# Kernel tuning notes

Hardware: AMD Instinct MI355X
Metric: run time of the kernel (lower is better)

## Reference

```python
import jax, jax.numpy as jnp
import numpy as np

WS = [2048, 4096, 8192]
RS = [1, 2, 4]
OFFSET = 0
NEG = -1e30


def _causal_attn(xseg, Wq, Wk, Wv, Wo):
    """xseg: (b, s, m, c). Returns (out (b,s,m,c), denom (b,s,m)) where denom is
    the softmax denominator sum_j exp(score_ij) per query (computed stably via lse)."""
    c = xseg.shape[-1]
    m = xseg.shape[-2]
    q = jnp.einsum('bsmc,cd->bsmd', xseg, Wq)
    k = jnp.einsum('bsmc,cd->bsmd', xseg, Wk)
    v = jnp.einsum('bsmc,cd->bsmd', xseg, Wv)
    scores = jnp.einsum('bsid,bsjd->bsij', q, k) / jnp.sqrt(jnp.asarray(c, xseg.dtype))
    causal = jnp.tril(jnp.ones((m, m), dtype=bool))
    scores = jnp.where(causal, scores, NEG)
    lse = jax.nn.logsumexp(scores, axis=-1)            # (b,s,m)
    p = jnp.exp(scores - lse[..., None])               # softmax
    o = jnp.einsum('bsij,bsjd->bsid', p, v)
    o = jnp.einsum('bsid,dc->bsic', o, Wo)
    return o, jnp.exp(lse)


def setup_inputs() -> dict:
    key = jax.random.key(0)
    kx, kq, kk, kv, ko = jax.random.split(key, 5)
    b, n, c = 4, 8192, 128
    scale = 1.0 / np.sqrt(c)  # keep activations O(1) so exp(lse) stays finite
    return {
        'x': jax.random.normal(kx, (b, n, c), dtype=jnp.float32),
        'Wq': jax.random.normal(kq, (c, c), dtype=jnp.float32) * scale,
        'Wk': jax.random.normal(kk, (c, c), dtype=jnp.float32) * scale,
        'Wv': jax.random.normal(kv, (c, c), dtype=jnp.float32) * scale,
        'Wo': jax.random.normal(ko, (c, c), dtype=jnp.float32) * scale,
    }


def reference(x, Wq, Wk, Wv, Wo):
    b, n, c = x.shape
    denom_sums = jnp.zeros((b, n), dtype=x.dtype)
    branches = []
    for w, r in zip(WS, RS):
        s = n // w
        # gather dilated tokens within each segment: (b, s, m, c)
        xr = x.reshape(b, s, w, c)[:, :, OFFSET::r, :]
        m = xr.shape[2]
        o, d = _causal_attn(xr, Wq, Wk, Wv, Wo)
        # global positions of the gathered tokens, flattened over (segment, within-seg)
        idx = (jnp.arange(s)[:, None] * w + OFFSET + r * jnp.arange(m)[None, :]).reshape(-1)
        d_flat = d.reshape(b, s * m)
        o_flat = o.reshape(b, s * m, c)
        denom_sums = denom_sums.at[:, idx].add(d_flat)
        branches.append((idx, o_flat, d_flat))
    out = jnp.zeros_like(x)
    for idx, o_flat, d_flat in branches:
        alpha = d_flat / denom_sums[:, idx]             # (b, s*m)
        out = out.at[:, idx].add(o_flat * alpha[..., None])
    return out
```

## Files before the change

kernel.cpp:

```cpp
#include <hip/hip_runtime.h>
#include <hip/hip_bf16.h>

typedef __attribute__((ext_vector_type(8))) __bf16 bf16x8;
typedef __attribute__((ext_vector_type(4))) float f32x4;
typedef __attribute__((ext_vector_type(8))) unsigned short u16x8;

#define DEVI __device__ __forceinline__
#define MFMA(a,b,c) __builtin_amdgcn_mfma_f32_16x16x32_bf16((a),(b),(c),0,0,0)
#define EXP2F(x) __builtin_exp2f(x)
#define LOG2F(x) __builtin_log2f(x)

DEVI unsigned short f2bf(float f){ __bf16 h = (__bf16)f; return __builtin_bit_cast(unsigned short, h); }
DEVI float bf2f(unsigned short u){ unsigned int x = ((unsigned int)u) << 16; return __builtin_bit_cast(float, x); }
DEVI bf16x8 ld_bf8(const void* p){ u16x8 u = *(const u16x8*)p; return __builtin_bit_cast(bf16x8, u); }
DEVI f32x4 splat4(float x){ f32x4 v = {x,x,x,x}; return v; }
DEVI f32x4 vmax4(f32x4 a, f32x4 b){
  f32x4 r;
  #pragma unroll
  for (int i=0;i<4;++i) r[i]=fmaxf(a[i],b[i]);
  return r;
}
DEVI void gload_lds16(const void* g, void* l){
  void* g2 = const_cast<void*>(g);
  __builtin_amdgcn_global_load_lds((__attribute__((address_space(1))) void*)g2,
                                   (__attribute__((address_space(3))) void*)l, 16, 0, 0);
}
#if __has_builtin(__builtin_amdgcn_permlane16_swap) && __has_builtin(__builtin_amdgcn_permlane32_swap)
DEVI float wavemax_hi(float x){
  unsigned int xu = __builtin_bit_cast(unsigned int, x);
  auto r1 = __builtin_amdgcn_permlane16_swap(xu, xu, false, false);
  float m = fmaxf(__builtin_bit_cast(float, (unsigned int)r1[0]),
                  __builtin_bit_cast(float, (unsigned int)r1[1]));
  unsigned int mu = __builtin_bit_cast(unsigned int, m);
  auto r2 = __builtin_amdgcn_permlane32_swap(mu, mu, false, false);
  return fmaxf(__builtin_bit_cast(float, (unsigned int)r2[0]),
               __builtin_bit_cast(float, (unsigned int)r2[1]));
}
#else
DEVI float wavemax_hi(float x){
  x = fmaxf(x, __shfl_xor(x, 16, 64));
  x = fmaxf(x, __shfl_xor(x, 32, 64));
  return x;
}
#endif

__device__ const unsigned int SCHED[30] = {
  0x100C000Bu, 0x110C0C0Bu, 0x050C0005u, 0x1C0B0A0Fu, 0x1D0B150Fu,
  0x0E0B000Au, 0x0F0B0B0Au, 0x1B0A000Fu, 0x180A000Eu, 0x190A0A0Eu,
  0x1A0A140Eu, 0x170A120Du, 0x0C0A0009u, 0x0D0A0A09u, 0x040A0004u,
  0x1509000Du, 0x1609090Du, 0x1309080Cu, 0x1409110Cu, 0x0A090008u,
  0x0B090908u, 0x1208000Cu, 0x08080007u, 0x09080807u, 0x03080003u,
  0x06070006u, 0x07070706u, 0x02060002u, 0x01040001u, 0x00020000u
};
__device__ const int CB[16] = {0,1,2,3,4,5,6,8,10,12,14,16,18,21,24,27};

__global__ __launch_bounds__(256) void k_prep(const float* __restrict__ Wq, const float* __restrict__ Wk,
                                              const float* __restrict__ Wv, const float* __restrict__ Wo,
                                              unsigned short* __restrict__ wT){
  int i = blockIdx.x*256 + threadIdx.x;
  int mat = i >> 14, col = (i >> 7) & 127, k = i & 127;
  const float* W = (mat==0)?Wq:(mat==1)?Wk:(mat==2)?Wv:Wo;
  float v = W[k*128 + col];
  if (mat == 0) v *= 0.12754245006257017f;
  wT[i] = f2bf(v);
}

__global__ __launch_bounds__(512) void k_qkv(const float* __restrict__ x, const unsigned short* __restrict__ wT,
                                             unsigned short* __restrict__ Qo, unsigned short* __restrict__ Ko,
                                             unsigned short* __restrict__ VT0, unsigned short* __restrict__ VT1,
                                             unsigned short* __restrict__ VT2){
  __shared__ unsigned short Tl[128*130];
  const int tid=threadIdx.x, lane=tid&63, wid=tid>>6, ll=lane&15, hi=lane>>4;
  const int row0g = blockIdx.x*128;
  const long row0 = (long)row0g + wid*16;
  bf16x8 a[4];
  {
    const float* xr = x + (row0 + ll)*128 + hi*8;
    #pragma unroll
    for (int ks=0;ks<4;++ks){
      f32x4 f0 = *(const f32x4*)(const void*)(xr + ks*32);
      f32x4 f1 = *(const f32x4*)(const void*)(xr + ks*32 + 4);
      u16x8 u;
      #pragma unroll
      for (int j=0;j<4;++j){ u[j]=f2bf(f0[j]); u[j+4]=f2bf(f1[j]); }
      a[ks] = __builtin_bit_cast(bf16x8, u);
    }
  }
  #pragma unroll
  for (int m3=0;m3<3;++m3){
    const unsigned short* wp = wT + m3*16384 + ll*128 + hi*8;
    #pragma unroll
    for (int nt=0;nt<8;++nt){
      f32x4 acc=splat4(0.f);
      #pragma unroll
      for (int ks=0;ks<4;++ks){
        bf16x8 b = ld_bf8(wp + nt*2048 + ks*32);
        acc = MFMA(a[ks], b, acc);
      }
      if (m3 < 2){
        unsigned short* outp = (m3==0)?Qo:Ko;
        #pragma unroll
        for (int r=0;r<4;++r)
          outp[(row0 + hi*4 + r)*128 + nt*16 + ll] = f2bf(acc[r]);
      } else {
        #pragma unroll
        for (int r=0;r<4;++r)
          Tl[(wid*16 + hi*4 + r)*130 + nt*16 + ll] = f2bf(acc[r]);
      }
    }
  }
  __syncthreads();
  int tk = 2*lane;
  int pp0 = (tk>>5)*32 + ((tk>>4)&1)*4 + ((tk&15)>>2)*8 + (tk&3);
  #pragma unroll 4
  for (int p=0;p<16;++p){
    int d = wid*16 + p;
    unsigned int w0 = (unsigned int)Tl[(2*lane)*130 + d] | ((unsigned int)Tl[(2*lane+1)*130 + d] << 16);
    *(unsigned int*)(VT0 + (long)d*32768 + row0g + pp0) = w0;
    if (lane < 32){
      unsigned int w1 = (unsigned int)Tl[(4*lane)*130 + d] | ((unsigned int)Tl[(4*lane+2)*130 + d] << 16);
      *(unsigned int*)(VT1 + (long)d*16384 + (row0g>>1) + pp0) = w1;
    }
    if (lane < 16){
      unsigned int w2 = (unsigned int)Tl[(8*lane)*130 + d] | ((unsigned int)Tl[(8*lane+4)*130 + d] << 16);
      *(unsigned int*)(VT2 + (long)d*8192 + (row0g>>2) + pp0) = w2;
    }
  }
}

__global__ __launch_bounds__(256,3) void k_attn(
    const unsigned short* __restrict__ Qg, const unsigned short* __restrict__ Kg,
    const unsigned short* __restrict__ VT0, const unsigned short* __restrict__ VT1,
    const unsigned short* __restrict__ VT2,
    unsigned short* __restrict__ OP, float* __restrict__ LP){
  __shared__ unsigned char smem[49152];

  const int tid=threadIdx.x, lane=tid&63, wid=tid>>6, ll=lane&15, hi=lane>>4;

  int x = blockIdx.x & 7;
  int i = blockIdx.x >> 3;
  int sid, r;
  if (i < 60){
    r = i >> 2; int k = i & 3;
    if (k < 3){ sid = 3*x + k; }
    else { sid = 24 + (x >> 1); if (x & 1) r += 15; }
  } else {
    int t = i - 60; r = 15 + t/3; sid = 3*x + t%3;
  }
  unsigned int e = SCHED[r];
  int qb   = (int)(e & 255u);
  int t032 = (int)((e >> 8) & 255u) * 2;
  int n32  = (int)((e >> 16) & 255u) * 2;
  int slot = (int)(e >> 24);
  int br, bb, seg;
  if (sid < 16){ br=0; bb=sid>>2; seg=sid&3; }
  else if (sid < 24){ br=1; bb=(sid-16)>>1; seg=(sid-16)&1; }
  else { br=2; bb=sid-24; seg=0; }
  const int rstr = 1 << br;
  const long g0 = (long)bb*8192 + (long)seg*(2048 << br);
  const int P = sid*30 + slot;
  const unsigned short* VTb = (br==0)?VT0:(br==1)?VT1:VT2;
  const int NC = 32768 >> br;
  const int rb0 = (int)(g0 >> br);

  const int qrow_w = qb*128 + wid*32;

  bf16x8 aq[2][4];
  #pragma unroll
  for (int mt=0;mt<2;++mt){
    long gq = g0 + (long)rstr*(qrow_w + mt*16 + ll);
    const unsigned short* qp = Qg + gq*128 + hi*8;
    #pragma unroll
    for (int ks=0;ks<4;++ks) aq[mt][ks] = ld_bf8(qp + ks*32);
  }

  f32x4 o[2][8];
  #pragma unroll
  for (int mt=0;mt<2;++mt){
    #pragma unroll
    for (int dt=0;dt<8;++dt) o[mt][dt]=splat4(0.f);
  }
  float mrun[2], lrun[2];
  mrun[0]=mrun[1]=-1e30f; lrun[0]=lrun[1]=0.f;

  const int m7 = ll & 7;
  int koffs[4];
  #pragma unroll
  for (int ks=0;ks<4;++ks) koffs[ks] = ll*256 + (((ks*4 + hi) ^ m7) * 16);
  const int voffb = ll*64 + (((hi + (ll >> 1)) & 3) * 16);

  const long kadv = (long)rstr*32*128;
  const unsigned short* ksrc0 = Kg + (g0 + (long)rstr*((long)t032*32 + wid*8 + hi))*128 + ((ll ^ hi) * 8);
  const unsigned short* ksrc1 = Kg + (g0 + (long)rstr*((long)t032*32 + wid*8 + 4 + hi))*128 + ((ll ^ (4 + hi)) * 8);
  const int d0_ = tid >> 2,        s0_ = tid & 3,        ga_ = (s0_ - (d0_ >> 1)) & 3;
  const int d1_ = (256+tid) >> 2,  s1_ = tid & 3,        gb_ = (s1_ - (d1_ >> 1)) & 3;
  const unsigned short* vsrc0 = VTb + (long)d0_*NC + rb0 + t032*32 + ga_*8;
  const unsigned short* vsrc1 = VTb + (long)d1_*NC + rb0 + t032*32 + gb_*8;

#define STAGE(bslot)                                                                   \
  {                                                                                    \
    unsigned char* Kb = smem + (bslot)*8192;                                           \
    unsigned char* Vb = smem + 24576 + (bslot)*8192;                                   \
    gload_lds16((const void*)ksrc0, (void*)(Kb + wid*2048));                           \
    gload_lds16((const void*)ksrc1, (void*)(Kb + wid*2048 + 1024));                    \
    gload_lds16((const void*)vsrc0, (void*)(Vb + wid*1024));                           \
    gload_lds16((const void*)vsrc1, (void*)(Vb + 4096 + wid*1024));                    \
    ksrc0 += kadv; ksrc1 += kadv; vsrc0 += 32; vsrc1 += 32;                            \
  }

  STAGE(0);
  STAGE(1);

  for (int it=0; it<n32; ++it){
    const int kt = t032 + it;
    if (it + 1 < n32){
      asm volatile("s_waitcnt vmcnt(4) lgkmcnt(0)" ::: "memory");
    } else {
      asm volatile("s_waitcnt vmcnt(0) lgkmcnt(0)" ::: "memory");
    }
    __builtin_amdgcn_s_barrier();
    __builtin_amdgcn_sched_barrier(0);

    if (it + 2 < n32){
      STAGE((it + 2) % 3);
    }

    if (kt*32 <= qrow_w + 31){
      unsigned char* Kc = smem + (it % 3)*8192;
      unsigned char* Vc = smem + 24576 + (it % 3)*8192;
      f32x4 s[2][2];
      #pragma unroll
      for (int mt=0;mt<2;++mt){
        #pragma unroll
        for (int nt=0;nt<2;++nt) s[mt][nt]=splat4(0.f);
      }
      #pragma unroll
      for (int nt=0;nt<2;++nt){
        #pragma unroll
        for (int ks=0;ks<4;++ks){
          bf16x8 bk = ld_bf8(Kc + koffs[ks] + nt*4096);
          s[0][nt] = MFMA(bk, aq[0][ks], s[0][nt]);
          s[1][nt] = MFMA(bk, aq[1][ks], s[1][nt]);
        }
      }
      if (kt*32 + 31 > qrow_w){
        #pragma unroll
        for (int mt=0;mt<2;++mt){
          int qrow = qrow_w + mt*16 + ll;
          #pragma unroll
          for (int nt=0;nt<2;++nt){
            int kvcol = kt*32 + nt*16 + hi*4;
            #pragma unroll
            for (int rr=0;rr<4;++rr) if (kvcol + rr > qrow) s[mt][nt][rr] = -1e30f;
          }
        }
      }
      #pragma unroll
      for (int mt=0;mt<2;++mt){
        f32x4 t4 = vmax4(s[mt][0], s[mt][1]);
        float mloc = fmaxf(fmaxf(t4[0],t4[1]), fmaxf(t4[2],t4[3]));
        mloc = wavemax_hi(mloc);
        bool upd = __any(mloc > mrun[mt] + 8.0f);
        if (upd){
          float mnew = fmaxf(mrun[mt], mloc);
          float sc = EXP2F(mrun[mt] - mnew);
          mrun[mt] = mnew;
          lrun[mt] *= sc;
          f32x4 scv;
          #pragma unroll
          for (int rr=0;rr<4;++rr) scv[rr] = __shfl(sc, hi*4 + rr, 64);
          #pragma unroll
          for (int dt=0;dt<8;++dt) o[mt][dt] = o[mt][dt]*scv;
        }
        f32x4 tsum = splat4(0.f);
        #pragma unroll
        for (int nt=0;nt<2;++nt){
          #pragma unroll
          for (int rr=0;rr<4;++rr) s[mt][nt][rr] = EXP2F(s[mt][nt][rr] - mrun[mt]);
          tsum += s[mt][nt];
        }
        lrun[mt] += (tsum[0]+tsum[1]) + (tsum[2]+tsum[3]);
      }
      bf16x8 pa[2];
      #pragma unroll
      for (int mt=0;mt<2;++mt){
        u16x8 up;
        #pragma unroll
        for (int rr=0;rr<4;++rr){
          up[rr]   = f2bf(s[mt][0][rr]);
          up[4+rr] = f2bf(s[mt][1][rr]);
        }
        pa[mt] = __builtin_bit_cast(bf16x8, up);
      }
      #pragma unroll
      for (int dt=0;dt<8;++dt){
        bf16x8 bv = ld_bf8(Vc + voffb + dt*1024);
        o[0][dt] = MFMA(pa[0], bv, o[0][dt]);
        o[1][dt] = MFMA(pa[1], bv, o[1][dt]);
      }
    }
  }
#undef STAGE

  unsigned short* op = OP + (long)P*16384;
  float* lp = LP + (long)P*128;
  #pragma unroll
  for (int mt=0;mt<2;++mt){
    float l = lrun[mt];
    l += __shfl_xor(l, 16, 64);
    l += __shfl_xor(l, 32, 64);
    float invs = 1.f / l;
    f32x4 iv;
    #pragma unroll
    for (int rr=0;rr<4;++rr) iv[rr] = __shfl(invs, hi*4 + rr, 64);
    #pragma unroll
    for (int dt=0;dt<8;++dt){
      f32x4 res = o[mt][dt]*iv;
      #pragma unroll
      for (int rr=0;rr<4;++rr){
        int qloc = wid*32 + mt*16 + hi*4 + rr;
        op[qloc*128 + dt*16 + ll] = f2bf(res[rr]);
      }
    }
    float lse = mrun[mt] + LOG2F(l);
    if (lane < 16){
      lp[wid*32 + mt*16 + lane] = lse;
    }
  }
}

__global__ __launch_bounds__(256) void k_comb(
    const unsigned short* __restrict__ OP, const float* __restrict__ LP,
    const unsigned short* __restrict__ wT, float* __restrict__ out){
  __shared__ float Wl[9*32];
  __shared__ unsigned short Tl[32*136];
  const int tid = threadIdx.x;
  const long G0 = (long)blockIdx.x * 32;
  const int bb = (int)(G0 >> 13);
  const int P0 = (int)(G0 & 8191);

  int pb[3], bn[3], qlb[3];
  {
    int sid0 = bb*4 + (P0 >> 11); int qb0 = (P0 & 2047) >> 7;
    pb[0] = sid0*30 + CB[qb0]; bn[0] = (qb0<6)?1:(qb0<12)?2:3; qlb[0] = P0 & 127;
    int p1b = P0 >> 1; int sid1 = 16 + bb*2 + (p1b >> 11); int qb1 = (p1b & 2047) >> 7;
    pb[1] = sid1*30 + CB[qb1]; bn[1] = (qb1<6)?1:(qb1<12)?2:3; qlb[1] = p1b & 127;
    int p2b = P0 >> 2; int sid2 = 24 + bb; int qb2 = p2b >> 7;
    pb[2] = sid2*30 + CB[qb2]; bn[2] = (qb2<6)?1:(qb2<12)?2:3; qlb[2] = p2b & 127;
  }

  if (tid < 32){
    int i = tid;
    float Lx[9];
    #pragma unroll
    for (int b=0;b<3;++b){
      bool pv = (i & ((1<<b)-1)) == 0;
      int ql = qlb[b] + (i >> b);
      #pragma unroll
      for (int c=0;c<3;++c){
        bool v = pv && (c < bn[b]);
        Lx[b*3+c] = v ? LP[(pb[b]+c)*128 + ql] : -1e30f;
      }
    }
    float mx = -1e30f;
    #pragma unroll
    for (int s=0;s<9;++s) mx = fmaxf(mx, Lx[s]);
    float W[9]; float wsum = 0.f;
    #pragma unroll
    for (int b=0;b<3;++b){
      bool pv = (i & ((1<<b)-1)) == 0;
      #pragma unroll
      for (int c=0;c<3;++c){
        bool v = pv && (c < bn[b]);
        W[b*3+c] = v ? EXP2F(Lx[b*3+c] - mx) : 0.f;
        wsum += W[b*3+c];
      }
    }
    float inv = 1.f / wsum;
    #pragma unroll
    for (int s=0;s<9;++s) Wl[s*32 + i] = W[s] * inv;
  }
  __syncthreads();

  {
    const int ch = tid & 15;
    const int r0 = tid >> 4;
    #pragma unroll
    for (int p=0;p<2;++p){
      int row = p*16 + r0;
      float y[8];
      #pragma unroll
      for (int j=0;j<8;++j) y[j] = 0.f;
      #pragma unroll
      for (int b=0;b<3;++b){
        if ((row & ((1<<b)-1)) == 0){
          int opr = qlb[b] + (row >> b);
          for (int c=0;c<bn[b];++c){
            float wgt = Wl[(b*3+c)*32 + row];
            const unsigned short* pp = OP + (long)(pb[b]+c)*16384 + opr*128 + ch*8;
            u16x8 u = *(const u16x8*)(const void*)pp;
            #pragma unroll
            for (int j=0;j<8;++j) y[j] += wgt * bf2f(u[j]);
          }
        }
      }
      u16x8 o;
      #pragma unroll
      for (int j=0;j<8;++j) o[j] = f2bf(y[j]);
      *(u16x8*)(void*)(Tl + row*136 + ch*8) = o;
    }
  }
  __syncthreads();

  {
    const int wv = tid >> 6, lane = tid & 63, ll = lane & 15, hi = lane >> 4;
    bf16x8 a[2][4];
    #pragma unroll
    for (int mt=0;mt<2;++mt){
      #pragma unroll
      for (int ks=0;ks<4;++ks)
        a[mt][ks] = ld_bf8(Tl + (mt*16 + ll)*136 + ks*32 + hi*8);
    }
    const unsigned short* wp = wT + 3*16384 + ll*128 + hi*8;
    #pragma unroll
    for (int t=0;t<2;++t){
      int nt = wv*2 + t;
      f32x4 acc0=splat4(0.f), acc1=splat4(0.f);
      #pragma unroll
      for (int ks=0;ks<4;++ks){
        bf16x8 b = ld_bf8(wp + nt*2048 + ks*32);
        acc0 = MFMA(a[0][ks], b, acc0);
        acc1 = MFMA(a[1][ks], b, acc1);
      }
      #pragma unroll
      for (int rr=0;rr<4;++rr){
        out[(G0 + hi*4 + rr)*128 + nt*16 + ll]      = acc0[rr];
        out[(G0 + 16 + hi*4 + rr)*128 + nt*16 + ll] = acc1[rr];
      }
    }
  }
}

extern "C" void kernel_launch(void* const* d_in, const int* in_sizes, int n_in,
                              void* d_out, int out_size, void* d_ws, size_t ws_size,
                              hipStream_t stream){
  const float* x  = (const float*)d_in[0];
  const float* Wq = (const float*)d_in[1];
  const float* Wk = (const float*)d_in[2];
  const float* Wv = (const float*)d_in[3];
  const float* Wo = (const float*)d_in[4];
  char* ws = (char*)d_ws;
  unsigned short* wT  = (unsigned short*)(ws);
  unsigned short* Q   = (unsigned short*)(ws + 131072);
  unsigned short* K   = (unsigned short*)(ws + 8519680);
  unsigned short* VT0 = (unsigned short*)(ws + 16908288);
  unsigned short* VT1 = (unsigned short*)(ws + 25296896);
  unsigned short* VT2 = (unsigned short*)(ws + 29491200);
  unsigned short* OP  = (unsigned short*)(ws + 31588352);
  float* LP           = (float*)(ws + 59113472);
  k_prep<<<256, 256, 0, stream>>>(Wq, Wk, Wv, Wo, wT);
  k_qkv <<<256, 512, 0, stream>>>(x, wT, Q, K, VT0, VT1, VT2);
  k_attn<<<840, 256, 0, stream>>>(Q, K, VT0, VT1, VT2, OP, LP);
  k_comb<<<1024, 256, 0, stream>>>(OP, LP, wT, (float*)d_out);
}
```

Measured before the change: 104.4 us.

## Use 64-wide KV tiles with double buffering instead of 32-wide triple buffering

Each main-loop iteration now processes 64 keys instead of 32, so there are half as many barriers and softmax rescale steps per KV sweep. The LDS ring changes from three 8 KB K/V stages to two 16 KB stages, and the V tile layout and swizzle are reworked for 64-column rows. The wait now drains all outstanding loads each iteration rather than keeping one stage in flight, so load/compute overlap is shallower. Occupancy is lowered to 2 blocks per CU and causal-diagonal masking waste grows with the coarser tile.

```diff
diff --git a/kernel.cpp b/kernel.cpp
--- a/kernel.cpp
+++ b/kernel.cpp
@@ -128,12 +128,12 @@
   }
 }
 
-__global__ __launch_bounds__(256,3) void k_attn(
+__global__ __launch_bounds__(256,2) void k_attn(
     const unsigned short* __restrict__ Qg, const unsigned short* __restrict__ Kg,
     const unsigned short* __restrict__ VT0, const unsigned short* __restrict__ VT1,
     const unsigned short* __restrict__ VT2,
     unsigned short* __restrict__ OP, float* __restrict__ LP){
-  __shared__ unsigned char smem[49152];
+  __shared__ unsigned char smem[65536];
 
   const int tid=threadIdx.x, lane=tid&63, wid=tid>>6, ll=lane&15, hi=lane>>4;
 
@@ -149,8 +149,8 @@
   }
   unsigned int e = SCHED[r];
   int qb   = (int)(e & 255u);
-  int t032 = (int)((e >> 8) & 255u) * 2;
-  int n32  = (int)((e >> 16) & 255u) * 2;
+  int t064 = (int)((e >> 8) & 255u);
+  int n64  = (int)((e >> 16) & 255u);
   int slot = (int)(e >> 24);
   int br, bb, seg;
   if (sid < 16){ br=0; bb=sid>>2; seg=sid&3; }
@@ -187,55 +187,56 @@
   int koffs[4];
   #pragma unroll
   for (int ks=0;ks<4;++ks) koffs[ks] = ll*256 + (((ks*4 + hi) ^ m7) * 16);
-  const int voffb = ll*64 + (((hi + (ll >> 1)) & 3) * 16);
-
-  const long kadv = (long)rstr*32*128;
-  const unsigned short* ksrc0 = Kg + (g0 + (long)rstr*((long)t032*32 + wid*8 + hi))*128 + ((ll ^ hi) * 8);
-  const unsigned short* ksrc1 = Kg + (g0 + (long)rstr*((long)t032*32 + wid*8 + 4 + hi))*128 + ((ll ^ (4 + hi)) * 8);
-  const int d0_ = tid >> 2,        s0_ = tid & 3,        ga_ = (s0_ - (d0_ >> 1)) & 3;
-  const int d1_ = (256+tid) >> 2,  s1_ = tid & 3,        gb_ = (s1_ - (d1_ >> 1)) & 3;
-  const unsigned short* vsrc0 = VTb + (long)d0_*NC + rb0 + t032*32 + ga_*8;
-  const unsigned short* vsrc1 = VTb + (long)d1_*NC + rb0 + t032*32 + gb_*8;
+  const int voff0 = ll*128 + (((hi + (ll >> 1)) & 7) * 16);
+  const int voff1 = ll*128 + (((4 + hi + (ll >> 1)) & 7) * 16);
+
+  const long kadv   = (long)rstr*64*128;
+  const long kstep2 = (long)rstr*8*128;
+  const unsigned short* ksrc0 = Kg + (g0 + (long)rstr*((long)t064*64 + wid*16 + hi))*128 + ((ll ^ hi) * 8);
+  const unsigned short* ksrc1 = Kg + (g0 + (long)rstr*((long)t064*64 + wid*16 + 4 + hi))*128 + ((ll ^ (4 + hi)) * 8);
+  const int dv = tid >> 3;
+  const int gv = ((tid & 7) - ((tid >> 4) & 7)) & 7;
+  const unsigned short* vsrcB = VTb + (long)dv*NC + rb0 + t064*64 + gv*8;
+  const long vstep = (long)32*NC;
 
 #define STAGE(bslot)                                                                   \
   {                                                                                    \
-    unsigned char* Kb = smem + (bslot)*8192;                                           \
-    unsigned char* Vb = smem + 24576 + (bslot)*8192;                                   \
-    gload_lds16((const void*)ksrc0, (void*)(Kb + wid*2048));                           \
-    gload_lds16((const void*)ksrc1, (void*)(Kb + wid*2048 + 1024));                    \
-    gload_lds16((const void*)vsrc0, (void*)(Vb + wid*1024));                           \
-    gload_lds16((const void*)vsrc1, (void*)(Vb + 4096 + wid*1024));                    \
-    ksrc0 += kadv; ksrc1 += kadv; vsrc0 += 32; vsrc1 += 32;                            \
+    unsigned char* Kb = smem + (bslot)*16384;                                          \
+    unsigned char* Vb = smem + 32768 + (bslot)*16384;                                  \
+    gload_lds16((const void*)ksrc0,            (void*)(Kb + wid*4096));                \
+    gload_lds16((const void*)ksrc1,            (void*)(Kb + wid*4096 + 1024));         \
+    gload_lds16((const void*)(ksrc0 + kstep2), (void*)(Kb + wid*4096 + 2048));         \
+    gload_lds16((const void*)(ksrc1 + kstep2), (void*)(Kb + wid*4096 + 3072));         \
+    gload_lds16((const void*)vsrcB,              (void*)(Vb + wid*1024));              \
+    gload_lds16((const void*)(vsrcB + vstep),    (void*)(Vb + 4096 + wid*1024));       \
+    gload_lds16((const void*)(vsrcB + 2*vstep),  (void*)(Vb + 8192 + wid*1024));       \
+    gload_lds16((const void*)(vsrcB + 3*vstep),  (void*)(Vb + 12288 + wid*1024));      \
+    ksrc0 += kadv; ksrc1 += kadv; vsrcB += 64;                                         \
   }
 
   STAGE(0);
-  STAGE(1);
-
-  for (int it=0; it<n32; ++it){
-    const int kt = t032 + it;
-    if (it + 1 < n32){
-      asm volatile("s_waitcnt vmcnt(4) lgkmcnt(0)" ::: "memory");
-    } else {
-      asm volatile("s_waitcnt vmcnt(0) lgkmcnt(0)" ::: "memory");
-    }
+
+  for (int it=0; it<n64; ++it){
+    const int kt = t064 + it;
+    asm volatile("s_waitcnt vmcnt(0) lgkmcnt(0)" ::: "memory");
     __builtin_amdgcn_s_barrier();
     __builtin_amdgcn_sched_barrier(0);
 
-    if (it + 2 < n32){
-      STAGE((it + 2) % 3);
-    }
-
-    if (kt*32 <= qrow_w + 31){
-      unsigned char* Kc = smem + (it % 3)*8192;
-      unsigned char* Vc = smem + 24576 + (it % 3)*8192;
-      f32x4 s[2][2];
+    if (it + 1 < n64){
+      STAGE((it + 1) & 1);
+    }
+
+    if (kt*64 <= qrow_w + 31){
+      unsigned char* Kc = smem + (it & 1)*16384;
+      unsigned char* Vc = smem + 32768 + (it & 1)*16384;
+      f32x4 s[2][4];
       #pragma unroll
       for (int mt=0;mt<2;++mt){
         #pragma unroll
-        for (int nt=0;nt<2;++nt) s[mt][nt]=splat4(0.f);
-      }
-      #pragma unroll
-      for (int nt=0;nt<2;++nt){
+        for (int nt=0;nt<4;++nt) s[mt][nt]=splat4(0.f);
+      }
+      #pragma unroll
+      for (int nt=0;nt<4;++nt){
         #pragma unroll
         for (int ks=0;ks<4;++ks){
           bf16x8 bk = ld_bf8(Kc + koffs[ks] + nt*4096);
@@ -243,21 +244,22 @@
           s[1][nt] = MFMA(bk, aq[1][ks], s[1][nt]);
         }
       }
-      if (kt*32 + 31 > qrow_w){
+      if (kt*64 + 63 > qrow_w){
         #pragma unroll
         for (int mt=0;mt<2;++mt){
           int qrow = qrow_w + mt*16 + ll;
           #pragma unroll
-          for (int nt=0;nt<2;++nt){
-            int kvcol = kt*32 + nt*16 + hi*4;
+          for (int nt=0;nt<4;++nt){
+            int kvcol = kt*64 + nt*16 + hi*4;
             #pragma unroll
             for (int rr=0;rr<4;++rr) if (kvcol + rr > qrow) s[mt][nt][rr] = -1e30f;
           }
         }
       }
+      bf16x8 pa[2][2];
       #pragma unroll
       for (int mt=0;mt<2;++mt){
-        f32x4 t4 = vmax4(s[mt][0], s[mt][1]);
+        f32x4 t4 = vmax4(vmax4(s[mt][0], s[mt][1]), vmax4(s[mt][2], s[mt][3]));
         float mloc = fmaxf(fmaxf(t4[0],t4[1]), fmaxf(t4[2],t4[3]));
         mloc = wavemax_hi(mloc);
         bool upd = __any(mloc > mrun[mt] + 8.0f);
@@ -274,29 +276,31 @@
         }
         f32x4 tsum = splat4(0.f);
         #pragma unroll
-        for (int nt=0;nt<2;++nt){
+        for (int nt=0;nt<4;++nt){
           #pragma unroll
           for (int rr=0;rr<4;++rr) s[mt][nt][rr] = EXP2F(s[mt][nt][rr] - mrun[mt]);
           tsum += s[mt][nt];
         }
         lrun[mt] += (tsum[0]+tsum[1]) + (tsum[2]+tsum[3]);
-      }
-      bf16x8 pa[2];
-      #pragma unroll
-      for (int mt=0;mt<2;++mt){
-        u16x8 up;
-        #pragma unroll
-        for (int rr=0;rr<4;++rr){
-          up[rr]   = f2bf(s[mt][0][rr]);
-          up[4+rr] = f2bf(s[mt][1][rr]);
-        }
-        pa[mt] = __builtin_bit_cast(bf16x8, up);
+        #pragma unroll
+        for (int h=0;h<2;++h){
+          u16x8 up;
+          #pragma unroll
+          for (int rr=0;rr<4;++rr){
+            up[rr]   = f2bf(s[mt][h*2][rr]);
+            up[4+rr] = f2bf(s[mt][h*2+1][rr]);
+          }
+          pa[mt][h] = __builtin_bit_cast(bf16x8, up);
+        }
       }
       #pragma unroll
       for (int dt=0;dt<8;++dt){
-        bf16x8 bv = ld_bf8(Vc + voffb + dt*1024);
-        o[0][dt] = MFMA(pa[0], bv, o[0][dt]);
-        o[1][dt] = MFMA(pa[1], bv, o[1][dt]);
+        bf16x8 bv0 = ld_bf8(Vc + voff0 + dt*2048);
+        bf16x8 bv1 = ld_bf8(Vc + voff1 + dt*2048);
+        o[0][dt] = MFMA(pa[0][0], bv0, o[0][dt]);
+        o[1][dt] = MFMA(pa[1][0], bv0, o[1][dt]);
+        o[0][dt] = MFMA(pa[0][1], bv1, o[0][dt]);
+        o[1][dt] = MFMA(pa[1][1], bv1, o[1][dt]);
       }
     }
   }
```

New measurement: 108.0 us. +3.4%, slower.
